# Kernel optimization log

Hardware: AMD Instinct MI355X
Metric: run time of the kernel (lower is better)

Reference implementation:

```python
import jax, jax.numpy as jnp
import numpy as np

N_ITER = 10   # inference() default
LR = 0.1      # inference() default


def setup_inputs() -> dict:
    key = jax.random.key(0)
    ks = jax.random.split(key, 7)
    dims = [1024, 2048, 2048, 1024]
    B = 4096
    inp = {"x": jax.random.normal(ks[0], (B, dims[0]), dtype=jnp.float32)}
    # params ~ randn * 0.1 as in the torch __init__
    for l, (d_in, d_out) in enumerate(zip(dims[:-1], dims[1:])):
        inp[f"V{l}"] = jax.random.normal(ks[1 + l], (d_in, d_out), dtype=jnp.float32) * 0.1
        inp[f"W{l}"] = jax.random.normal(ks[4 + l], (d_out, d_in), dtype=jnp.float32) * 0.1
    return inp


def _energy(states, V, W):
    # E = sum_l mse(x[l+1] @ W[l], x[l]) + mse(x[l] @ V[l], x[l+1]), mean over all elems
    E = jnp.float32(0.0)
    for l in range(len(V)):
        v_down = states[l + 1] @ W[l]
        E = E + jnp.mean(jnp.square(v_down - states[l]))
        v_up = states[l] @ V[l]
        E = E + jnp.mean(jnp.square(v_up - states[l + 1]))
    return E


def _inference(x, V, W):
    # feedforward init of latent states
    states = [x]
    for l in range(len(V)):
        states.append(states[-1] @ V[l])
    hidden = tuple(states[1:])  # all latents are free since y is None

    grad_fn = jax.grad(lambda h: _energy((x,) + h, V, W))

    def step(h, _):
        g = grad_fn(h)
        h = tuple(hi - LR * gi for hi, gi in zip(h, g))
        return h, None

    hidden, _ = jax.lax.scan(step, hidden, None, length=N_ITER)
    return hidden


def reference(x, V0, V1, V2, W0, W1, W2):
    V = (V0, V1, V2)
    W = (W0, W1, W2)
    hidden = _inference(x, V, W)
    # final-layer state after iterative bidirectional inference (the PCN prediction)
    return hidden[-1]
```

## Files before the change

### kernel.cpp

```cpp
#include <hip/hip_runtime.h>
#include <hip/hip_bf16.h>

typedef unsigned short u16;
typedef __bf16 bf16x8 __attribute__((ext_vector_type(8)));
typedef float f32x4 __attribute__((ext_vector_type(4)));

__device__ __forceinline__ u16 f2bf(float f) {
    unsigned u = __builtin_bit_cast(unsigned, f);
    unsigned r = (u + 0x7fffu + ((u >> 16) & 1u)) >> 16;
    return (u16)r;
}

#define GLDS16(g, l)                                                      \
    __builtin_amdgcn_global_load_lds(                                     \
        (const __attribute__((address_space(1))) void*)(g),               \
        (__attribute__((address_space(3))) void*)(l), 16, 0, 0)

__global__ __launch_bounds__(256) void prep_convert(const float* __restrict__ x,
                                                    u16* __restrict__ xb,
                                                    const float* __restrict__ V0,
                                                    u16* __restrict__ V0b) {
    int i0 = blockIdx.x * 512 + threadIdx.x;
#pragma unroll
    for (int p = 0; p < 2; ++p) {
        int i = i0 + p * 256;
        const float* s; u16* d; int j;
        if (i < 1048576) { s = x; d = xb; j = i; }
        else { s = V0; d = V0b; j = i - 1048576; }
        float4 v = ((const float4*)s)[j];
        ushort4 o; o.x = f2bf(v.x); o.y = f2bf(v.y); o.z = f2bf(v.z); o.w = f2bf(v.w);
        ((ushort4*)d)[j] = o;
    }
}

__global__ __launch_bounds__(256) void prep_transpose(const float* __restrict__ V1,
                                                      u16* __restrict__ V1t,
                                                      const float* __restrict__ V2,
                                                      u16* __restrict__ V2t) {
    __shared__ float tile[64][65];
    const int b = blockIdx.x;
    const float* src; u16* dst; int C, rt, ct;
    if (b < 1024) { src = V1; dst = V1t; C = 2048; rt = b >> 5; ct = b & 31; }
    else { int b2 = b - 1024; src = V2; dst = V2t; C = 1024; rt = b2 >> 4; ct = b2 & 15; }
    const int r0 = rt * 64, c0 = ct * 64;
    const int t = threadIdx.x;
    const int trow = t >> 4;
    const int tc4 = t & 15;

#pragma unroll
    for (int p = 0; p < 4; ++p) {
        int r = p * 16 + trow;
        float4 v = *(const float4*)&src[(size_t)(r0 + r) * C + c0 + tc4 * 4];
        tile[r][tc4 * 4 + 0] = v.x; tile[r][tc4 * 4 + 1] = v.y;
        tile[r][tc4 * 4 + 2] = v.z; tile[r][tc4 * 4 + 3] = v.w;
    }
    __syncthreads();
#pragma unroll
    for (int p = 0; p < 4; ++p) {
        int c = p * 16 + trow;
        int rr = tc4 * 4;
        ushort4 o;
        o.x = f2bf(tile[rr + 0][c]); o.y = f2bf(tile[rr + 1][c]);
        o.z = f2bf(tile[rr + 2][c]); o.w = f2bf(tile[rr + 3][c]);
        *(ushort4*)&dst[(size_t)(c0 + c) * 2048 + r0 + rr] = o;
    }
}

__global__ __launch_bounds__(512) void gemm_bt(const u16* __restrict__ A,
                                               const u16* __restrict__ Bt,
                                               u16* __restrict__ Cpart,
                                               int M, int N, int Ktot, int Kc) {
    __shared__ u16 sA[2][128 * 32];
    __shared__ u16 sB[2][128 * 32];

    const int t = threadIdx.x;
    const int lane = t & 63;
    const int w = t >> 6;
    const int wr = w >> 2, wc = w & 3;
    const int l15 = lane & 15, l4 = lane >> 4;
    const int row0 = blockIdx.y * 128, col0 = blockIdx.x * 128;
    const int kbase = blockIdx.z * Kc;

    f32x4 acc[4][2] = {};

    const int sr = t >> 2;
    const int sk = (t & 3) * 8;
    const u16* Ab = A  + (size_t)(row0 + sr) * Ktot + kbase + sk;
    const u16* Bb = Bt + (size_t)(col0 + sr) * Ktot + kbase + sk;

    GLDS16(Ab, &sA[0][t * 8]);
    GLDS16(Bb, &sB[0][t * 8]);
    asm volatile("s_waitcnt vmcnt(0)" ::: "memory");
    __builtin_amdgcn_s_barrier();

    const int nK = Kc >> 5;
    int cur = 0;
    for (int kt = 0; kt < nK; ++kt) {
        if (kt + 1 < nK) {
            GLDS16(Ab + (kt + 1) * 32, &sA[cur ^ 1][t * 8]);
            GLDS16(Bb + (kt + 1) * 32, &sB[cur ^ 1][t * 8]);
        }

        bf16x8 af[4], bfr[2];
#pragma unroll
        for (int m = 0; m < 4; ++m)
            af[m] = *(const bf16x8*)&sA[cur][(wr * 64 + m * 16 + l15) * 32 + l4 * 8];
#pragma unroll
        for (int n = 0; n < 2; ++n)
            bfr[n] = *(const bf16x8*)&sB[cur][(wc * 32 + n * 16 + l15) * 32 + l4 * 8];
#pragma unroll
        for (int m = 0; m < 4; ++m)
#pragma unroll
            for (int n = 0; n < 2; ++n)
                acc[m][n] = __builtin_amdgcn_mfma_f32_16x16x32_bf16(af[m], bfr[n], acc[m][n], 0, 0, 0);

        asm volatile("s_waitcnt vmcnt(0)" ::: "memory");
        __builtin_amdgcn_s_barrier();
        cur ^= 1;
    }

    const size_t zoff = (size_t)blockIdx.z * M * N;
#pragma unroll
    for (int m = 0; m < 4; ++m)
#pragma unroll
        for (int n = 0; n < 2; ++n) {
            int r = row0 + wr * 64 + m * 16 + l4 * 4;
            int c = col0 + wc * 32 + n * 16 + l15;
#pragma unroll
            for (int j = 0; j < 4; ++j)
                Cpart[zoff + (size_t)(r + j) * N + c] = f2bf(acc[m][n][j]);
        }
}

template <int KS, int F32OUT>
__global__ __launch_bounds__(256) void reduce_parts(const u16* __restrict__ part,
                                                    void* __restrict__ out, int mn) {
    int i = blockIdx.x * 256 + threadIdx.x;
    int n8 = mn >> 3;
    if (i >= n8) return;
    float s[8] = {0, 0, 0, 0, 0, 0, 0, 0};
#pragma unroll
    for (int z = 0; z < KS; ++z) {
        uint4 v = ((const uint4*)(part + (size_t)z * mn))[i];
        unsigned a0 = v.x, a1 = v.y, a2 = v.z, a3 = v.w;
        s[0] += __builtin_bit_cast(float, a0 << 16);
        s[1] += __builtin_bit_cast(float, a0 & 0xffff0000u);
        s[2] += __builtin_bit_cast(float, a1 << 16);
        s[3] += __builtin_bit_cast(float, a1 & 0xffff0000u);
        s[4] += __builtin_bit_cast(float, a2 << 16);
        s[5] += __builtin_bit_cast(float, a2 & 0xffff0000u);
        s[6] += __builtin_bit_cast(float, a3 << 16);
        s[7] += __builtin_bit_cast(float, a3 & 0xffff0000u);
    }
    if (F32OUT) {
        float4 o0 = {s[0], s[1], s[2], s[3]};
        float4 o1 = {s[4], s[5], s[6], s[7]};
        ((float4*)out)[2 * i] = o0;
        ((float4*)out)[2 * i + 1] = o1;
    } else {
        uint4 o;
        o.x = (unsigned)f2bf(s[0]) | ((unsigned)f2bf(s[1]) << 16);
        o.y = (unsigned)f2bf(s[2]) | ((unsigned)f2bf(s[3]) << 16);
        o.z = (unsigned)f2bf(s[4]) | ((unsigned)f2bf(s[5]) << 16);
        o.w = (unsigned)f2bf(s[6]) | ((unsigned)f2bf(s[7]) << 16);
        ((uint4*)out)[i] = o;
    }
}

extern "C" void kernel_launch(void* const* d_in, const int* in_sizes, int n_in,
                              void* d_out, int out_size, void* d_ws, size_t ws_size,
                              hipStream_t stream) {
    const float* x  = (const float*)d_in[0];
    const float* V0 = (const float*)d_in[1];
    const float* V1 = (const float*)d_in[3];
    const float* V2 = (const float*)d_in[5];

    char* ws = (char*)d_ws;
    u16* xb   = (u16*)(ws);
    u16* V0b  = (u16*)(ws + ((size_t)8 << 20));
    u16* V1t  = (u16*)(ws + ((size_t)12 << 20));
    u16* V2t  = (u16*)(ws + ((size_t)20 << 20));
    u16* P1   = (u16*)(ws + ((size_t)24 << 20));
    u16* P2t  = (u16*)(ws + ((size_t)28 << 20));
    u16* part = (u16*)(ws + ((size_t)30 << 20));

    prep_convert<<<3072, 256, 0, stream>>>(x, xb, V0, V0b);
    prep_transpose<<<1536, 256, 0, stream>>>(V1, V1t, V2, V2t);

    gemm_bt<<<dim3(16, 8, 4), 512, 0, stream>>>(V0b, V1t, part, 1024, 2048, 2048, 512);
    reduce_parts<4, 0><<<1024, 256, 0, stream>>>(part, P1, 1024 * 2048);

    gemm_bt<<<dim3(8, 8, 8), 512, 0, stream>>>(V2t, P1, part, 1024, 1024, 2048, 256);
    reduce_parts<8, 0><<<512, 256, 0, stream>>>(part, P2t, 1024 * 1024);

    gemm_bt<<<dim3(8, 32, 2), 512, 0, stream>>>(xb, P2t, part, 4096, 1024, 1024, 512);
    reduce_parts<2, 1><<<2048, 256, 0, stream>>>(part, d_out, 4096 * 1024);
}
```

Baseline: 81.43 us.

## Fuse prep kernels, merge x conversion into reduce, drop split-K for final GEMM

Combines V0 conversion with the V1/V2 transposes in one launch and moves the x-to-bf16 conversion into the first reduction kernel, cutting launch count. The last GEMM no longer uses split-K plus a separate reduction: a dedicated kernel with 128x64 tiles writes fp32 output directly, avoiding the bf16 partial write/read round trip and one launch. The direct GEMM has fewer MFMAs per B load and a full K loop per block, so it relies on more blocks for occupancy.

After: 75.47 us. -7.3%, faster.

```diff
diff --git a/kernel.cpp b/kernel.cpp
--- a/kernel.cpp
+++ b/kernel.cpp
@@ -16,34 +16,30 @@
         (const __attribute__((address_space(1))) void*)(g),               \
         (__attribute__((address_space(3))) void*)(l), 16, 0, 0)
 
-__global__ __launch_bounds__(256) void prep_convert(const float* __restrict__ x,
-                                                    u16* __restrict__ xb,
-                                                    const float* __restrict__ V0,
-                                                    u16* __restrict__ V0b) {
-    int i0 = blockIdx.x * 512 + threadIdx.x;
-#pragma unroll
-    for (int p = 0; p < 2; ++p) {
-        int i = i0 + p * 256;
-        const float* s; u16* d; int j;
-        if (i < 1048576) { s = x; d = xb; j = i; }
-        else { s = V0; d = V0b; j = i - 1048576; }
-        float4 v = ((const float4*)s)[j];
-        ushort4 o; o.x = f2bf(v.x); o.y = f2bf(v.y); o.z = f2bf(v.z); o.w = f2bf(v.w);
-        ((ushort4*)d)[j] = o;
-    }
-}
-
-__global__ __launch_bounds__(256) void prep_transpose(const float* __restrict__ V1,
-                                                      u16* __restrict__ V1t,
-                                                      const float* __restrict__ V2,
-                                                      u16* __restrict__ V2t) {
+__global__ __launch_bounds__(256) void prep(const float* __restrict__ V0,
+                                            u16* __restrict__ V0b,
+                                            const float* __restrict__ V1,
+                                            u16* __restrict__ V1t,
+                                            const float* __restrict__ V2,
+                                            u16* __restrict__ V2t) {
     __shared__ float tile[64][65];
-    const int b = blockIdx.x;
+    const int b = blockIdx.x, t = threadIdx.x;
+    if (b < 1024) {
+        int i0 = b * 512 + t;
+#pragma unroll
+        for (int p = 0; p < 2; ++p) {
+            int j = i0 + p * 256;
+            float4 v = ((const float4*)V0)[j];
+            ushort4 o; o.x = f2bf(v.x); o.y = f2bf(v.y); o.z = f2bf(v.z); o.w = f2bf(v.w);
+            ((ushort4*)V0b)[j] = o;
+        }
+        return;
+    }
+    const int b2 = b - 1024;
     const float* src; u16* dst; int C, rt, ct;
-    if (b < 1024) { src = V1; dst = V1t; C = 2048; rt = b >> 5; ct = b & 31; }
-    else { int b2 = b - 1024; src = V2; dst = V2t; C = 1024; rt = b2 >> 4; ct = b2 & 15; }
+    if (b2 < 1024) { src = V1; dst = V1t; C = 2048; rt = b2 >> 5; ct = b2 & 31; }
+    else { int b3 = b2 - 1024; src = V2; dst = V2t; C = 1024; rt = b3 >> 4; ct = b3 & 15; }
     const int r0 = rt * 64, c0 = ct * 64;
-    const int t = threadIdx.x;
     const int trow = t >> 4;
     const int tc4 = t & 15;
 
@@ -132,15 +128,53 @@
         }
 }
 
-template <int KS, int F32OUT>
-__global__ __launch_bounds__(256) void reduce_parts(const u16* __restrict__ part,
-                                                    void* __restrict__ out, int mn) {
+__global__ __launch_bounds__(256) void reduce1_xconv(const u16* __restrict__ part,
+                                                     u16* __restrict__ P1,
+                                                     const float* __restrict__ x,
+                                                     u16* __restrict__ xb) {
+    const int b = blockIdx.x, t = threadIdx.x;
+    if (b < 1024) {
+        const int mn = 1024 * 2048;
+        int i = b * 256 + t;
+        float s[8] = {0, 0, 0, 0, 0, 0, 0, 0};
+#pragma unroll
+        for (int z = 0; z < 4; ++z) {
+            uint4 v = ((const uint4*)(part + (size_t)z * mn))[i];
+            unsigned a0 = v.x, a1 = v.y, a2 = v.z, a3 = v.w;
+            s[0] += __builtin_bit_cast(float, a0 << 16);
+            s[1] += __builtin_bit_cast(float, a0 & 0xffff0000u);
+            s[2] += __builtin_bit_cast(float, a1 << 16);
+            s[3] += __builtin_bit_cast(float, a1 & 0xffff0000u);
+            s[4] += __builtin_bit_cast(float, a2 << 16);
+            s[5] += __builtin_bit_cast(float, a2 & 0xffff0000u);
+            s[6] += __builtin_bit_cast(float, a3 << 16);
+            s[7] += __builtin_bit_cast(float, a3 & 0xffff0000u);
+        }
+        uint4 o;
+        o.x = (unsigned)f2bf(s[0]) | ((unsigned)f2bf(s[1]) << 16);
+        o.y = (unsigned)f2bf(s[2]) | ((unsigned)f2bf(s[3]) << 16);
+        o.z = (unsigned)f2bf(s[4]) | ((unsigned)f2bf(s[5]) << 16);
+        o.w = (unsigned)f2bf(s[6]) | ((unsigned)f2bf(s[7]) << 16);
+        ((uint4*)P1)[i] = o;
+        return;
+    }
+    int i0 = (b - 1024) * 512 + t;
+#pragma unroll
+    for (int p = 0; p < 2; ++p) {
+        int j = i0 + p * 256;
+        float4 v = ((const float4*)x)[j];
+        ushort4 o; o.x = f2bf(v.x); o.y = f2bf(v.y); o.z = f2bf(v.z); o.w = f2bf(v.w);
+        ((ushort4*)xb)[j] = o;
+    }
+}
+
+__global__ __launch_bounds__(256) void reduce2(const u16* __restrict__ part,
+                                               u16* __restrict__ P2t) {
+    const int mn = 1024 * 1024;
     int i = blockIdx.x * 256 + threadIdx.x;
-    int n8 = mn >> 3;
-    if (i >= n8) return;
     float s[8] = {0, 0, 0, 0, 0, 0, 0, 0};
 #pragma unroll
-    for (int z = 0; z < KS; ++z) {
+    for (int z = 0; z < 8; ++z) {
         uint4 v = ((const uint4*)(part + (size_t)z * mn))[i];
         unsigned a0 = v.x, a1 = v.y, a2 = v.z, a3 = v.w;
         s[0] += __builtin_bit_cast(float, a0 << 16);
@@ -152,18 +186,68 @@
         s[6] += __builtin_bit_cast(float, a3 << 16);
         s[7] += __builtin_bit_cast(float, a3 & 0xffff0000u);
     }
-    if (F32OUT) {
-        float4 o0 = {s[0], s[1], s[2], s[3]};
-        float4 o1 = {s[4], s[5], s[6], s[7]};
-        ((float4*)out)[2 * i] = o0;
-        ((float4*)out)[2 * i + 1] = o1;
-    } else {
-        uint4 o;
-        o.x = (unsigned)f2bf(s[0]) | ((unsigned)f2bf(s[1]) << 16);
-        o.y = (unsigned)f2bf(s[2]) | ((unsigned)f2bf(s[3]) << 16);
-        o.z = (unsigned)f2bf(s[4]) | ((unsigned)f2bf(s[5]) << 16);
-        o.w = (unsigned)f2bf(s[6]) | ((unsigned)f2bf(s[7]) << 16);
-        ((uint4*)out)[i] = o;
+    uint4 o;
+    o.x = (unsigned)f2bf(s[0]) | ((unsigned)f2bf(s[1]) << 16);
+    o.y = (unsigned)f2bf(s[2]) | ((unsigned)f2bf(s[3]) << 16);
+    o.z = (unsigned)f2bf(s[4]) | ((unsigned)f2bf(s[5]) << 16);
+    o.w = (unsigned)f2bf(s[6]) | ((unsigned)f2bf(s[7]) << 16);
+    ((uint4*)P2t)[i] = o;
+}
+
+__global__ __launch_bounds__(512) void gemm3_direct(const u16* __restrict__ A,
+                                                    const u16* __restrict__ Bt,
+                                                    float* __restrict__ C) {
+    __shared__ u16 sA[2][128 * 32];
+    __shared__ u16 sB[2][64 * 32];
+
+    const int t = threadIdx.x;
+    const int lane = t & 63;
+    const int w = t >> 6;
+    const int wr = w >> 2, wc = w & 3;
+    const int l15 = lane & 15, l4 = lane >> 4;
+    const int row0 = blockIdx.y * 128, col0 = blockIdx.x * 64;
+
+    f32x4 acc[4];
+#pragma unroll
+    for (int m = 0; m < 4; ++m) acc[m] = (f32x4){0.f, 0.f, 0.f, 0.f};
+
+    const bool doB = t < 256;
+    const u16* Abase = A  + (size_t)(row0 + (t >> 2)) * 1024 + (t & 3) * 8;
+    const u16* Bbase = Bt + (size_t)(col0 + ((t & 255) >> 2)) * 1024 + (t & 3) * 8;
+
+    GLDS16(Abase, &sA[0][t * 8]);
+    if (doB) GLDS16(Bbase, &sB[0][(t & 255) * 8]);
+    asm volatile("s_waitcnt vmcnt(0)" ::: "memory");
+    __builtin_amdgcn_s_barrier();
+
+    int cur = 0;
+    for (int kt = 0; kt < 32; ++kt) {
+        if (kt + 1 < 32) {
+            GLDS16(Abase + (kt + 1) * 32, &sA[cur ^ 1][t * 8]);
+            if (doB) GLDS16(Bbase + (kt + 1) * 32, &sB[cur ^ 1][(t & 255) * 8]);
+        }
+
+        bf16x8 af[4], bfr;
+#pragma unroll
+        for (int m = 0; m < 4; ++m)
+            af[m] = *(const bf16x8*)&sA[cur][(wr * 64 + m * 16 + l15) * 32 + l4 * 8];
+        bfr = *(const bf16x8*)&sB[cur][(wc * 16 + l15) * 32 + l4 * 8];
+#pragma unroll
+        for (int m = 0; m < 4; ++m)
+            acc[m] = __builtin_amdgcn_mfma_f32_16x16x32_bf16(af[m], bfr, acc[m], 0, 0, 0);
+
+        asm volatile("s_waitcnt vmcnt(0)" ::: "memory");
+        __builtin_amdgcn_s_barrier();
+        cur ^= 1;
+    }
+
+#pragma unroll
+    for (int m = 0; m < 4; ++m) {
+        int r = row0 + wr * 64 + m * 16 + l4 * 4;
+        int c = col0 + wc * 16 + l15;
+#pragma unroll
+        for (int j = 0; j < 4; ++j)
+            C[(size_t)(r + j) * 1024 + c] = acc[m][j];
     }
 }
 
@@ -184,15 +268,15 @@
     u16* P2t  = (u16*)(ws + ((size_t)28 << 20));
     u16* part = (u16*)(ws + ((size_t)30 << 20));
 
-    prep_convert<<<3072, 256, 0, stream>>>(x, xb, V0, V0b);
-    prep_transpose<<<1536, 256, 0, stream>>>(V1, V1t, V2, V2t);
+    prep<<<2560, 256, 0, stream>>>(V0, V0b, V1, V1t, V2, V2t);
 
     gemm_bt<<<dim3(16, 8, 4), 512, 0, stream>>>(V0b, V1t, part, 1024, 2048, 2048, 512);
-    reduce_parts<4, 0><<<1024, 256, 0, stream>>>(part, P1, 1024 * 2048);
+
+    reduce1_xconv<<<3072, 256, 0, stream>>>(part, P1, x, xb);
 
     gemm_bt<<<dim3(8, 8, 8), 512, 0, stream>>>(V2t, P1, part, 1024, 1024, 2048, 256);
-    reduce_parts<8, 0><<<512, 256, 0, stream>>>(part, P2t, 1024 * 1024);
-
-    gemm_bt<<<dim3(8, 32, 2), 512, 0, stream>>>(xb, P2t, part, 4096, 1024, 1024, 512);
-    reduce_parts<2, 1><<<2048, 256, 0, stream>>>(part, d_out, 4096 * 1024);
-}
+
+    reduce2<<<512, 256, 0, stream>>>(part, P2t);
+
+    gemm3_direct<<<dim3(16, 32), 512, 0, stream>>>(xb, P2t, (float*)d_out);
+}
```
